# Kernel tuning notes

Measured on AMD Instinct MI355X. Metric: run time of the kernel, lower is better.

Reference implementation:

```python
import jax, jax.numpy as jnp
import numpy as np

P = 16
PW = P // 2 + 1  # 9, rfft width


def setup_inputs() -> dict:
    key = jax.random.key(0)
    ks = jax.random.split(key, 5)
    B, C, H, W = 128, 3, 224, 224
    E = 768
    N = (H // P) * (W // P)  # 196
    return {
        "x": jax.random.normal(ks[0], (B, C, H, W), dtype=jnp.float32),
        "freq_weight_h": jnp.ones((P,), dtype=jnp.float32),
        "freq_weight_w": jnp.ones((PW,), dtype=jnp.float32),
        "proj_w": jax.random.normal(ks[1], (E, C * P * PW), dtype=jnp.float32) * 0.02,
        "proj_b": jnp.zeros((E,), dtype=jnp.float32),
        "cls_token": jax.random.normal(ks[2], (1, 1, E), dtype=jnp.float32),
        "pos_emb": jax.random.normal(ks[3], (1, N + 1, E), dtype=jnp.float32),
    }


def reference(x, freq_weight_h, freq_weight_w, proj_w, proj_b, cls_token, pos_emb):
    B, C, H, W = x.shape
    nH, nW = H // P, W // P
    N = nH * nW
    # unfold into non-overlapping PxP patches: (B, C, N, P, P)
    patches = x.reshape(B, C, nH, P, nW, P).transpose(0, 1, 2, 4, 3, 5)
    patches = patches.reshape(B, C, N, P, P)
    # rfft2 with ortho norm, keep real part: (B, C, N, P, PW)
    x_fft = jnp.fft.rfft2(patches, norm="ortho").real
    # frequency reweighting
    x_fft = x_fft * freq_weight_h[None, None, None, :, None]
    x_fft = x_fft * freq_weight_w[None, None, None, None, :]
    # (B, N, C*P*PW)
    x_flat = x_fft.transpose(0, 2, 1, 3, 4).reshape(B, N, C * P * PW)
    # linear projection to embed_dim
    x_proj = jnp.einsum("bnf,ef->bne", x_flat, proj_w) + proj_b
    # prepend cls token, add position embeddings (dropout is eval/identity)
    cls = jnp.broadcast_to(cls_token, (B, 1, cls_token.shape[-1]))
    out = jnp.concatenate([cls, x_proj], axis=1) + pos_emb
    return out
```

## Files before the change

### kernel.cpp

```cpp
#include <hip/hip_runtime.h>
#include <hip/hip_bf16.h>

typedef __bf16 bf16;
typedef __attribute__((ext_vector_type(8))) __bf16 bf16x8;
typedef __attribute__((ext_vector_type(4))) float floatx4;

#define PP 16
#define PPW 9
#define CFEAT 432
#define EDIM 768
#define KDIM 768
#define NPAT 196
#define NBATCH 128
#define MROWS (NBATCH * NPAT)

#define NB_W 2304
#define NB_CLS 384
#define NB_UNF 9408
#define NB_PREP (NB_W + NB_CLS + NB_UNF)

__device__ inline void gload16(const void* g, void* l) {
  __builtin_amdgcn_global_load_lds(
      (const __attribute__((address_space(1))) void*)g,
      (__attribute__((address_space(3))) void*)l, 16, 0, 0);
}

__global__ __launch_bounds__(256) void prep_kernel(
    const float* __restrict__ x, const float* __restrict__ pw,
    const float* __restrict__ fwh, const float* __restrict__ fww,
    const float* __restrict__ cls, const float* __restrict__ pos,
    bf16* __restrict__ Wb, bf16* __restrict__ A, float* __restrict__ out) {
  const int blk = blockIdx.x;
  const int t = threadIdx.x;

  if (blk >= NB_W + NB_CLS) {
    const int i = (blk - NB_W - NB_CLS) * 256 + t;
    const int w8 = i % 28;
    const int tmp = i / 28;
    const int h = tmp % 224;
    const int tmp2 = tmp / 224;
    const int c = tmp2 % 3;
    const int b = tmp2 / 3;
    const float4 f0 = *reinterpret_cast<const float4*>(x + (size_t)i * 8);
    const float4 f1 = *reinterpret_cast<const float4*>(x + (size_t)i * 8 + 4);
    bf16x8 v;
    v[0] = (bf16)f0.x; v[1] = (bf16)f0.y; v[2] = (bf16)f0.z; v[3] = (bf16)f0.w;
    v[4] = (bf16)f1.x; v[5] = (bf16)f1.y; v[6] = (bf16)f1.z; v[7] = (bf16)f1.w;
    const int row = b * NPAT + (h >> 4) * 14 + (w8 >> 1);
    const int k = c * 256 + (h & 15) * 16 + (w8 & 1) * 8;
    *reinterpret_cast<bf16x8*>(A + (size_t)row * KDIM + k) = v;
  } else if (blk < NB_W) {
    __shared__ float s_pw[144];
    __shared__ float s_fh[16];
    __shared__ float s_fw[9];
    __shared__ float s_cos[16];
    const int e = blk / 3;
    const int c = blk % 3;
    if (t < 144) s_pw[t] = pw[e * CFEAT + c * 144 + t];
    if (t < 16) {
      s_fh[t] = fwh[t];
      s_cos[t] = cosf((float)t * 0.39269908169872414f);
    }
    if (t < 9) s_fw[t] = fww[t];
    __syncthreads();
    const int h = t >> 4, w = t & 15;
    float acc = 0.f;
#pragma unroll
    for (int u = 0; u < 16; ++u) {
      const float fh = s_fh[u];
      const int uh = (u * h) & 15;
#pragma unroll
      for (int v = 0; v < 9; ++v) {
        acc += s_pw[u * 9 + v] * s_fw[v] * s_cos[(uh + v * w) & 15] * fh;
      }
    }
    Wb[e * KDIM + c * 256 + t] = (bf16)(acc * 0.0625f);
  } else {
    const int idx = (blk - NB_W) * 256 + t;
    const int b = idx / 768;
    const int e = idx - b * 768;
    out[(size_t)b * 197 * 768 + e] = cls[e] + pos[e];
  }
}

__global__ __launch_bounds__(512) void gemm_256_kernel(
    const bf16* __restrict__ A, const bf16* __restrict__ Wb,
    const float* __restrict__ pb, const float* __restrict__ pos,
    float* __restrict__ out) {
  __shared__ __align__(16) bf16 sA[2][256 * 32];
  __shared__ __align__(16) bf16 sB[2][128 * 32];

  const int bid = blockIdx.x;
  const int xcd = bid & 7;
  const int idx = bid >> 3;
  const int wgid = (xcd < 4 ? xcd * 74 : 296 + (xcd - 4) * 73) + idx;
  const int mt = wgid / 6;
  const int nt = wgid - mt * 6;

  const int t = threadIdx.x;
  const int l = t & 63;
  const int wv = t >> 6;
  const int wm = wv >> 1;
  const int wn = wv & 1;
  const int lr = l & 15, lq = l >> 4;

  const bf16* gA0 = A + (size_t)(mt * 256 + (t >> 2)) * KDIM + (t & 3) * 8;
  const bf16* gA1 = A + (size_t)(mt * 256 + 128 + (t >> 2)) * KDIM + (t & 3) * 8;
  const bf16* gB0 = Wb + (size_t)(nt * 128 + (t >> 2)) * KDIM + (t & 3) * 8;
  const int lbase = wv * 512;

#define STAGE(buf, kts)                           \
  do {                                            \
    const int ko = (kts)*32;                      \
    gload16(gA0 + ko, &sA[buf][lbase]);           \
    gload16(gA1 + ko, &sA[buf][4096 + lbase]);    \
    gload16(gB0 + ko, &sB[buf][lbase]);           \
  } while (0)

  floatx4 acc[4][4];
#pragma unroll
  for (int i = 0; i < 4; ++i)
#pragma unroll
    for (int j = 0; j < 4; ++j) acc[i][j] = (floatx4){0.f, 0.f, 0.f, 0.f};

#define COMPUTE(buf)                                                        \
  do {                                                                      \
    bf16x8 af[4], bfr[4];                                                   \
    _Pragma("unroll") for (int mi = 0; mi < 4; ++mi) {                      \
      const int r = wm * 64 + mi * 16 + lr;                                 \
      af[mi] = *reinterpret_cast<const bf16x8*>(&sA[buf][r * 32 + lq * 8]); \
    }                                                                       \
    _Pragma("unroll") for (int ni = 0; ni < 4; ++ni) {                      \
      const int r = wn * 64 + ni * 16 + lr;                                 \
      bfr[ni] = *reinterpret_cast<const bf16x8*>(&sB[buf][r * 32 + lq * 8]);\
    }                                                                       \
    _Pragma("unroll") for (int mi = 0; mi < 4; ++mi)                        \
        _Pragma("unroll") for (int ni = 0; ni < 4; ++ni) acc[mi][ni] =      \
            __builtin_amdgcn_mfma_f32_16x16x32_bf16(af[mi], bfr[ni],        \
                                                    acc[mi][ni], 0, 0, 0);  \
  } while (0)

  STAGE(0, 0);
  __syncthreads();
  int cur = 0;
  for (int kt = 0; kt < 23; ++kt) {
    STAGE(cur ^ 1, kt + 1);
    COMPUTE(cur);
    __syncthreads();
    cur ^= 1;
  }
  COMPUTE(cur);
#undef STAGE
#undef COMPUTE

  float pbv[4];
#pragma unroll
  for (int ni = 0; ni < 4; ++ni)
    pbv[ni] = pb[nt * 128 + wn * 64 + ni * 16 + lr];

#pragma unroll
  for (int mi = 0; mi < 4; ++mi) {
#pragma unroll
    for (int j = 0; j < 4; ++j) {
      const unsigned m = wm * 64 + mi * 16 + lq * 4 + j;
      const unsigned Rr = mt * 256u + m;
      const unsigned b2 = Rr / 196u;
      const unsigned np2 = Rr - b2 * 196u;
      float* orow = out + ((size_t)b2 * 197 + 1 + np2) * 768;
      const float* prow = pos + (size_t)(1 + np2) * 768;
#pragma unroll
      for (int ni = 0; ni < 4; ++ni) {
        const int e = nt * 128 + wn * 64 + ni * 16 + lr;
        orow[e] = acc[mi][ni][j] + pbv[ni] + prow[e];
      }
    }
  }
}

extern "C" void kernel_launch(void* const* d_in, const int* in_sizes, int n_in,
                              void* d_out, int out_size, void* d_ws,
                              size_t ws_size, hipStream_t stream) {
  const float* x = (const float*)d_in[0];
  const float* fwh = (const float*)d_in[1];
  const float* fww = (const float*)d_in[2];
  const float* proj_w = (const float*)d_in[3];
  const float* proj_b = (const float*)d_in[4];
  const float* cls = (const float*)d_in[5];
  const float* pos = (const float*)d_in[6];
  float* out = (float*)d_out;

  const size_t needW = (size_t)EDIM * KDIM * sizeof(bf16);
  bf16* Wb = (bf16*)d_ws;
  bf16* A = (bf16*)((char*)d_ws + needW);

  prep_kernel<<<NB_PREP, 256, 0, stream>>>(x, proj_w, fwh, fww, cls, pos, Wb,
                                           A, out);
  gemm_256_kernel<<<588, 512, 0, stream>>>(A, Wb, proj_b, pos, out);
}
```

Measured before the change: 82.27 us.

## Shrink GEMM tile to 128x128 and load B fragments directly into registers

The GEMM moves from 256x128 tiles with 512 threads to 128x128 tiles with 256 threads, doubling the block count to 1176. The B operand is no longer staged through LDS: each wave loads its MFMA B fragments straight from global memory into a double-buffered register set, and the k-loop is fully unrolled in pairs. The block-to-tile swizzle is simplified to a uniform XCD mapping. This cuts LDS traffic and footprint and raises occupancy, at the cost of uncoalesced, latency-exposed global loads for B and more A re-reads across N tiles.

```diff
diff --git a/kernel.cpp b/kernel.cpp
--- a/kernel.cpp
+++ b/kernel.cpp
@@ -83,74 +83,88 @@
   }
 }
 
-__global__ __launch_bounds__(512) void gemm_256_kernel(
+__global__ __launch_bounds__(256) void gemm_bg_kernel(
     const bf16* __restrict__ A, const bf16* __restrict__ Wb,
     const float* __restrict__ pb, const float* __restrict__ pos,
     float* __restrict__ out) {
-  __shared__ __align__(16) bf16 sA[2][256 * 32];
-  __shared__ __align__(16) bf16 sB[2][128 * 32];
+  __shared__ __align__(16) bf16 sA[2][128 * 32];
 
   const int bid = blockIdx.x;
-  const int xcd = bid & 7;
-  const int idx = bid >> 3;
-  const int wgid = (xcd < 4 ? xcd * 74 : 296 + (xcd - 4) * 73) + idx;
-  const int mt = wgid / 6;
-  const int nt = wgid - mt * 6;
-
+  const int swz = (bid & 7) * 147 + (bid >> 3);
+  const int mt = swz / 6;
+  const int nt = swz - mt * 6;
   const int t = threadIdx.x;
   const int l = t & 63;
   const int wv = t >> 6;
-  const int wm = wv >> 1;
-  const int wn = wv & 1;
+  const int wm = wv >> 1, wn = wv & 1;
   const int lr = l & 15, lq = l >> 4;
 
-  const bf16* gA0 = A + (size_t)(mt * 256 + (t >> 2)) * KDIM + (t & 3) * 8;
-  const bf16* gA1 = A + (size_t)(mt * 256 + 128 + (t >> 2)) * KDIM + (t & 3) * 8;
-  const bf16* gB0 = Wb + (size_t)(nt * 128 + (t >> 2)) * KDIM + (t & 3) * 8;
+  const bf16* gA0 = A + (size_t)(mt * 128 + (t >> 2)) * KDIM + (t & 3) * 8;
+  const bf16* gA1 = gA0 + (size_t)64 * KDIM;
   const int lbase = wv * 512;
 
-#define STAGE(buf, kts)                           \
+  const bf16* baseB[4];
+#pragma unroll
+  for (int ni = 0; ni < 4; ++ni)
+    baseB[ni] =
+        Wb + (size_t)(nt * 128 + wn * 64 + ni * 16 + lr) * KDIM + lq * 8;
+
+#define STAGEA(buf, kts)                          \
   do {                                            \
     const int ko = (kts)*32;                      \
     gload16(gA0 + ko, &sA[buf][lbase]);           \
-    gload16(gA1 + ko, &sA[buf][4096 + lbase]);    \
-    gload16(gB0 + ko, &sB[buf][lbase]);           \
+    gload16(gA1 + ko, &sA[buf][2048 + lbase]);    \
   } while (0)
 
+#define LOADB(P, kts)                                              \
+  do {                                                             \
+    _Pragma("unroll") for (int ni = 0; ni < 4; ++ni) breg[P][ni] = \
+        *reinterpret_cast<const bf16x8*>(baseB[ni] + (kts)*32);    \
+  } while (0)
+
   floatx4 acc[4][4];
 #pragma unroll
   for (int i = 0; i < 4; ++i)
 #pragma unroll
     for (int j = 0; j < 4; ++j) acc[i][j] = (floatx4){0.f, 0.f, 0.f, 0.f};
 
-#define COMPUTE(buf)                                                        \
+  bf16x8 breg[2][4];
+
+#define COMPUTE(buf, P)                                                     \
   do {                                                                      \
-    bf16x8 af[4], bfr[4];                                                   \
+    bf16x8 af[4];                                                           \
     _Pragma("unroll") for (int mi = 0; mi < 4; ++mi) {                      \
       const int r = wm * 64 + mi * 16 + lr;                                 \
       af[mi] = *reinterpret_cast<const bf16x8*>(&sA[buf][r * 32 + lq * 8]); \
     }                                                                       \
-    _Pragma("unroll") for (int ni = 0; ni < 4; ++ni) {                      \
-      const int r = wn * 64 + ni * 16 + lr;                                 \
-      bfr[ni] = *reinterpret_cast<const bf16x8*>(&sB[buf][r * 32 + lq * 8]);\
-    }                                                                       \
     _Pragma("unroll") for (int mi = 0; mi < 4; ++mi)                        \
         _Pragma("unroll") for (int ni = 0; ni < 4; ++ni) acc[mi][ni] =      \
-            __builtin_amdgcn_mfma_f32_16x16x32_bf16(af[mi], bfr[ni],        \
+            __builtin_amdgcn_mfma_f32_16x16x32_bf16(af[mi], breg[P][ni],    \
                                                     acc[mi][ni], 0, 0, 0);  \
   } while (0)
 
-  STAGE(0, 0);
+  STAGEA(0, 0);
+  LOADB(0, 0);
   __syncthreads();
-  int cur = 0;
-  for (int kt = 0; kt < 23; ++kt) {
-    STAGE(cur ^ 1, kt + 1);
-    COMPUTE(cur);
+
+#pragma unroll
+  for (int it = 0; it < 11; ++it) {
+    STAGEA(1, 2 * it + 1);
+    LOADB(1, 2 * it + 1);
+    COMPUTE(0, 0);
     __syncthreads();
-    cur ^= 1;
+    STAGEA(0, 2 * it + 2);
+    LOADB(0, 2 * it + 2);
+    COMPUTE(1, 1);
+    __syncthreads();
   }
-  COMPUTE(cur);
-#undef STAGE
+  STAGEA(1, 23);
+  LOADB(1, 23);
+  COMPUTE(0, 0);
+  __syncthreads();
+  COMPUTE(1, 1);
+#undef STAGEA
+#undef LOADB
 #undef COMPUTE
 
   float pbv[4];
@@ -163,7 +177,7 @@
 #pragma unroll
     for (int j = 0; j < 4; ++j) {
       const unsigned m = wm * 64 + mi * 16 + lq * 4 + j;
-      const unsigned Rr = mt * 256u + m;
+      const unsigned Rr = mt * 128u + m;
       const unsigned b2 = Rr / 196u;
       const unsigned np2 = Rr - b2 * 196u;
       float* orow = out + ((size_t)b2 * 197 + 1 + np2) * 768;
@@ -195,5 +209,5 @@
 
   prep_kernel<<<NB_PREP, 256, 0, stream>>>(x, proj_w, fwh, fww, cls, pos, Wb,
                                            A, out);
-  gemm_256_kernel<<<588, 512, 0, stream>>>(A, Wb, proj_b, pos, out);
-}
+  gemm_bg_kernel<<<1176, 256, 0, stream>>>(A, Wb, proj_b, pos, out);
+}
```

Result: slower. 113.4 us (+37.8%).
